# Kernel optimization log

Hardware: AMD Instinct MI355X
Metric: run time of the kernel (lower is better)

Reference implementation:

```python
import jax, jax.numpy as jnp
import numpy as np

N_NODES = 50000


def _gcn_conv(x, row, col, W, b, n_nodes):
    """PyG GCNConv: symmetric-normalized scatter-add aggregation.
    row/col already include self-loops. x: [N, Fin], W: [Fin, Fout]."""
    h = x @ W  # [N, Fout]
    deg = jax.ops.segment_sum(jnp.ones(col.shape[0], x.dtype), col,
                              num_segments=n_nodes)  # in-degree incl. self-loops
    dis = jnp.where(deg > 0, jax.lax.rsqrt(deg), 0.0)  # deg^{-1/2}
    norm = dis[row] * dis[col]  # [E+N]
    msg = h[row] * norm[:, None]  # gather + scale, [E+N, Fout]
    out = jax.ops.segment_sum(msg, col, num_segments=n_nodes)  # scatter-add
    return out + b


def setup_inputs() -> dict:
    key = jax.random.key(0)
    k1, k2, k3, k4 = jax.random.split(key, 4)
    N, E, FIN, FH = N_NODES, 800000, 512, 512
    x = jax.random.normal(k1, (N, FIN), dtype=jnp.float32)
    edge_index = jax.random.randint(k2, (2, E), 0, N, dtype=jnp.int64)
    W1 = jax.random.normal(k3, (FIN, FH), dtype=jnp.float32) * (1.0 / np.sqrt(FIN))
    b1 = jnp.zeros((FH,), jnp.float32)
    W2 = jax.random.normal(k4, (FH, FH), dtype=jnp.float32) * (1.0 / np.sqrt(FH))
    b2 = jnp.zeros((FH,), jnp.float32)
    return {"x": x, "edge_index": edge_index, "W1": W1, "b1": b1,
            "W2": W2, "b2": b2}


def reference(x, edge_index, W1, b1, W2, b2):
    n = x.shape[0]
    loops = jnp.arange(n, dtype=edge_index.dtype)
    row = jnp.concatenate([edge_index[0], loops])  # sources
    col = jnp.concatenate([edge_index[1], loops])  # targets
    h = _gcn_conv(x, row, col, W1, b1, n)
    h = jax.nn.relu(h)
    return _gcn_conv(h, row, col, W2, b2, n)
```

## Files before the change

kernel.cpp:

```cpp
#include <hip/hip_runtime.h>
#include <hip/hip_bf16.h>

typedef short short8 __attribute__((ext_vector_type(8)));
typedef unsigned short u16x8 __attribute__((ext_vector_type(8)));
typedef float f32x4 __attribute__((ext_vector_type(4)));

#define AS1 __attribute__((address_space(1)))
#define AS3 __attribute__((address_space(3)))

__device__ __forceinline__ void gload16(const void* g, void* l) {
  __builtin_amdgcn_global_load_lds((AS1 void*)g, (AS3 void*)l, 16, 0, 0);
}

__device__ __forceinline__ unsigned short f2bf(float f) {
  unsigned u = __float_as_uint(f);
  u = (u + 0x7FFF + ((u >> 16) & 1)) >> 16;
  return (unsigned short)u;
}
__device__ __forceinline__ float bf2f(unsigned short u) {
  return __uint_as_float(((unsigned)u) << 16);
}

__global__ void prep_kernel(const float4* __restrict__ x4, ushort4* __restrict__ xb4, int n4,
                            const float* __restrict__ W1, unsigned short* __restrict__ W1t,
                            const float* __restrict__ W2, unsigned short* __restrict__ W2t) {
  const int nthr = gridDim.x * 256;
  for (int i = blockIdx.x * 256 + threadIdx.x; i < n4; i += nthr) {
    float4 v = x4[i];
    ushort4 o;
    o.x = f2bf(v.x); o.y = f2bf(v.y); o.z = f2bf(v.z); o.w = f2bf(v.w);
    xb4[i] = o;
  }
  for (int idx = blockIdx.x * 256 + threadIdx.x; idx < 512 * 512; idx += nthr) {
    const int k = idx >> 9, n = idx & 511;
    W1t[n * 512 + k] = f2bf(W1[idx]);
    W2t[n * 512 + k] = f2bf(W2[idx]);
  }
}

__global__ void detect64_kernel(const int* __restrict__ ei32, int* __restrict__ flag) {
  const int lane = threadIdx.x;
  const int v = ei32[2 * lane + 1];
  const unsigned long long m = __ballot(v != 0);
  if (lane == 0) *flag = (m == 0ull) ? 1 : 0;
}

__global__ void count_kernel(const int* __restrict__ ei32, const int* __restrict__ flag,
                             int* __restrict__ cnt4, int E, int qdiv) {
  int e = blockIdx.x * 256 + threadIdx.x;
  if (e >= E) return;
  const int is64 = *flag;
  const int r = is64 ? ei32[2 * e] : ei32[e];
  const int c = is64 ? ei32[2 * E + 2 * e] : ei32[E + e];
  int q = r / qdiv; q = q > 3 ? 3 : q;
  atomicAdd(&cnt4[c * 4 + q], 1);
}

__global__ void __launch_bounds__(1024) scan_bsum_kernel(const int* __restrict__ cnt,
                                                         int* __restrict__ bsum, int n) {
  __shared__ int ws[16];
  const int tid = threadIdx.x, lane = tid & 63, wid = tid >> 6;
  const int i = blockIdx.x * 1024 + tid;
  int x = (i < n) ? cnt[i] : 0;
#pragma unroll
  for (int d = 1; d < 64; d <<= 1) x += __shfl_xor(x, d, 64);
  if (lane == 0) ws[wid] = x;
  __syncthreads();
  if (tid == 0) {
    int s = 0;
#pragma unroll
    for (int w = 0; w < 16; ++w) s += ws[w];
    bsum[blockIdx.x] = s;
  }
}

__global__ void __launch_bounds__(1024) scan_boff_kernel(int* __restrict__ bsum,
                                                         int* __restrict__ total, int B) {
  __shared__ int ws[16];
  const int tid = threadIdx.x, lane = tid & 63, wid = tid >> 6;
  const int v = (tid < B) ? bsum[tid] : 0;
  int x = v;
#pragma unroll
  for (int d = 1; d < 64; d <<= 1) {
    int y = __shfl_up(x, d, 64);
    if (lane >= d) x += y;
  }
  if (lane == 63) ws[wid] = x;
  __syncthreads();
  if (tid < 16) {
    int wv = ws[tid];
    int wx = wv;
#pragma unroll
    for (int d = 1; d < 16; d <<= 1) {
      int y = __shfl_up(wx, d, 64);
      if (tid >= d) wx += y;
    }
    ws[tid] = wx - wv;
  }
  __syncthreads();
  const int excl = ws[wid] + (x - v);
  if (tid < B) bsum[tid] = excl;
  if (tid == B - 1) *total = excl + v;
}

__global__ void __launch_bounds__(1024) scan_fill_kernel(const int* __restrict__ cnt,
    const int* __restrict__ boff, int* __restrict__ ptr, int* __restrict__ cur,
    float* __restrict__ dis, int n) {
  __shared__ int ws[16];
  const int tid = threadIdx.x, lane = tid & 63, wid = tid >> 6;
  const int j = blockIdx.x * 1024 + tid;
  const int v = (j < n) ? cnt[j] : 0;
  int x = v;
#pragma unroll
  for (int d = 1; d < 64; d <<= 1) {
    int y = __shfl_up(x, d, 64);
    if (lane >= d) x += y;
  }
  if (lane == 63) ws[wid] = x;
  __syncthreads();
  if (tid < 16) {
    int wv = ws[tid];
    int wx = wv;
#pragma unroll
    for (int d = 1; d < 16; d <<= 1) {
      int y = __shfl_up(wx, d, 64);
      if (tid >= d) wx += y;
    }
    ws[tid] = wx - wv;
  }
  __syncthreads();
  const int v1 = __shfl_down(v, 1, 64);
  const int v2 = __shfl_down(v, 2, 64);
  const int v3 = __shfl_down(v, 3, 64);
  if (j < n) {
    const int excl = boff[blockIdx.x] + ws[wid] + (x - v);
    ptr[j] = excl;
    cur[j] = excl;
    if ((j & 3) == 0) dis[j >> 2] = rsqrtf((float)(v + v1 + v2 + v3 + 1));
  }
}

__global__ void fill_kernel(const int* __restrict__ ei32, const int* __restrict__ flag,
                            int* __restrict__ cur4, int* __restrict__ eidx, int E, int qdiv) {
  int e = blockIdx.x * 256 + threadIdx.x;
  if (e >= E) return;
  const int is64 = *flag;
  const int r = is64 ? ei32[2 * e] : ei32[e];
  const int c = is64 ? ei32[2 * E + 2 * e] : ei32[E + e];
  int q = r / qdiv; q = q > 3 ? 3 : q;
  const int pos = atomicAdd(&cur4[c * 4 + q], 1);
  eidx[pos] = r;
}

template <bool BA, bool BC>
__global__ void __launch_bounds__(256, 3) gemm_kernel(const unsigned short* __restrict__ A,
                                                      const unsigned short* __restrict__ Bt,
                                                      const float* __restrict__ dscale,
                                                      unsigned short* __restrict__ C, int M) {
  __shared__ alignas(128) unsigned short As[8192];
  __shared__ alignas(128) unsigned short Bs[8192];
  const int tid = threadIdx.x;
  const int wave = tid >> 6, lane = tid & 63;
  const int wm = wave >> 1, wn = wave & 1;

  const int nbm = (M + 127) >> 7;
  const int nwg = nbm * 4;
  const int orig = blockIdx.x;
  const int xcd = orig & 7;
  const int q8 = nwg >> 3, r8 = nwg & 7;
  const int wg = (xcd < r8 ? xcd * (q8 + 1) : r8 * (q8 + 1) + (xcd - r8) * q8) + (orig >> 3);
  const int bn = wg & 3;
  const int bm = wg >> 2;

  const int lr = lane >> 3, ls = lane & 7;
  const int fr = lane & 15, ks = lane >> 4;

  f32x4 acc[4][4] = {};

#define STAGE(KO)                                                                          \
  {                                                                                        \
    _Pragma("unroll") for (int i = 0; i < 4; ++i) {                                        \
      int ra = bm * 128 + i * 32 + wave * 8 + lr;                                          \
      ra = ra < M ? ra : M - 1;                                                            \
      const size_t aoff = BA ? ((size_t)(KO)*M + (size_t)ra * 64 + ((ls ^ (lr & 7)) << 3)) \
                             : ((size_t)ra * 512 + (KO) + ((ls ^ (lr & 7)) << 3));         \
      gload16(A + aoff, &As[(i * 32 + wave * 8) * 64]);                                    \
      const int rb = bn * 128 + i * 32 + wave * 8 + lr;                                    \
      gload16(Bt + (size_t)rb * 512 + (KO) + ((ls ^ (lr & 7)) << 3),                       \
              &Bs[(i * 32 + wave * 8) * 64]);                                              \
    }                                                                                      \
  }

  for (int kt = 0; kt < 8; ++kt) {
    if (kt) __syncthreads();
    STAGE(kt * 64)
    __syncthreads();

#pragma unroll
    for (int kk = 0; kk < 2; ++kk) {
      short8 af[4], bfg[4];
#pragma unroll
      for (int m = 0; m < 4; ++m) {
        const int tr = wm * 64 + m * 16 + fr;
        af[m] = *(const short8*)&As[tr * 64 + ((ks * 8 + kk * 32) ^ ((tr & 7) << 3))];
      }
#pragma unroll
      for (int n = 0; n < 4; ++n) {
        const int tb = wn * 64 + n * 16 + fr;
        bfg[n] = *(const short8*)&Bs[tb * 64 + ((ks * 8 + kk * 32) ^ ((tb & 7) << 3))];
      }
#pragma unroll
      for (int m = 0; m < 4; ++m)
#pragma unroll
        for (int n = 0; n < 4; ++n)
          acc[m][n] = __builtin_amdgcn_mfma_f32_16x16x32_bf16(af[m], bfg[n], acc[m][n], 0, 0, 0);
    }
  }
#undef STAGE

  const int rbase = bm * 128 + wm * 64 + (lane >> 4) * 4;
  const int cbase = bn * 128 + wn * 64 + (lane & 15);
  const size_t hseg = (size_t)M * 64;
#pragma unroll
  for (int m = 0; m < 4; ++m)
#pragma unroll
    for (int j = 0; j < 4; ++j) {
      const int r = rbase + m * 16 + j;
      if (r < M) {
        const float ds = dscale[r];
#pragma unroll
        for (int n = 0; n < 4; ++n) {
          const unsigned short val = f2bf(acc[m][n][j] * ds);
          if (BC) {
            const int col = cbase + n * 16;
            C[(size_t)(col >> 6) * hseg + (size_t)r * 64 + (col & 63)] = val;
          } else {
            C[(size_t)r * 512 + cbase + n * 16] = val;
          }
        }
      }
    }
}

template <bool FINAL>
__global__ void __launch_bounds__(256) agg_kernel(const unsigned short* __restrict__ h,
    const int* __restrict__ eidx, const int* __restrict__ ptr4, const float* __restrict__ dis,
    const float* __restrict__ bias, void* __restrict__ outv, int n) {
  const int tid = threadIdx.x;
  const int lane = tid & 63;
  const int slice = blockIdx.x & 7;
  const int g = lane >> 3;
  const int c = lane & 7;
  const int node = (int)(blockIdx.x >> 3) * 32 + (tid >> 6) * 8 + g;
  if (node >= n) return;

  const unsigned short* hs = h + (size_t)slice * ((size_t)n * 64);
  const int coff = c * 8;

  const int start = ptr4[node * 4], end = ptr4[node * 4 + 4];
  float acc[8] = {0, 0, 0, 0, 0, 0, 0, 0};

  int e = start;
  for (; e + 2 <= end; e += 2) {
    const int s0 = eidx[e], s1 = eidx[e + 1];
    const u16x8 v0 = *(const u16x8*)(hs + (size_t)(unsigned)s0 * 64 + coff);
    const u16x8 v1 = *(const u16x8*)(hs + (size_t)(unsigned)s1 * 64 + coff);
#pragma unroll
    for (int j = 0; j < 8; ++j) acc[j] += bf2f(v0[j]) + bf2f(v1[j]);
  }
  if (e < end) {
    const int s0 = eidx[e];
    const u16x8 v = *(const u16x8*)(hs + (size_t)(unsigned)s0 * 64 + coff);
#pragma unroll
    for (int j = 0; j < 8; ++j) acc[j] += bf2f(v[j]);
  }

  {
    const u16x8 v = *(const u16x8*)(hs + (size_t)node * 64 + coff);
#pragma unroll
    for (int j = 0; j < 8; ++j) acc[j] += bf2f(v[j]);
  }

  const float di = dis[node];
  const int fcol = slice * 64 + coff;
  float b[8];
  *(float4*)&b[0] = *(const float4*)(bias + fcol);
  *(float4*)&b[4] = *(const float4*)(bias + fcol + 4);

  if (FINAL) {
    float* out = (float*)outv;
    float4 o0, o1;
    o0.x = acc[0] * di + b[0]; o0.y = acc[1] * di + b[1];
    o0.z = acc[2] * di + b[2]; o0.w = acc[3] * di + b[3];
    o1.x = acc[4] * di + b[4]; o1.y = acc[5] * di + b[5];
    o1.z = acc[6] * di + b[6]; o1.w = acc[7] * di + b[7];
    *(float4*)(out + (size_t)node * 512 + fcol) = o0;
    *(float4*)(out + (size_t)node * 512 + fcol + 4) = o1;
  } else {
    unsigned short* out = (unsigned short*)outv;
    u16x8 o;
#pragma unroll
    for (int j = 0; j < 8; ++j) {
      const float t = acc[j] * di + b[j];
      o[j] = f2bf(t > 0.0f ? t : 0.0f);
    }
    *(u16x8*)(out + (size_t)slice * ((size_t)n * 64) + (size_t)node * 64 + coff) = o;
  }
}

extern "C" void kernel_launch(void* const* d_in, const int* in_sizes, int n_in,
                              void* d_out, int out_size, void* d_ws, size_t ws_size,
                              hipStream_t stream) {
  const float* x  = (const float*)d_in[0];
  const int*   ei = (const int*)d_in[1];
  const float* W1 = (const float*)d_in[2];
  const float* b1 = (const float*)d_in[3];
  const float* W2 = (const float*)d_in[4];
  const float* b2 = (const float*)d_in[5];
  float* out = (float*)d_out;

  const int M = in_sizes[0] / 512;
  const int E = in_sizes[1] / 2;
  const int qdiv = (M + 3) >> 2;

  auto alignup = [](size_t v) { return (v + 255) & ~(size_t)255; };
  char* p = (char*)d_ws;
  unsigned short* xb  = (unsigned short*)p; p += alignup((size_t)M * 512 * 2);
  unsigned short* h1b = (unsigned short*)p; p += alignup((size_t)M * 512 * 2);
  unsigned short* r1b = (unsigned short*)p; p += alignup((size_t)M * 512 * 2);
  unsigned short* w1b = (unsigned short*)p; p += alignup(512 * 512 * 2);
  unsigned short* w2b = (unsigned short*)p; p += alignup(512 * 512 * 2);
  float* dis = (float*)p; p += alignup((size_t)M * 4);
  int* ptr4  = (int*)p;   p += alignup(((size_t)M * 4 + 1) * 4);
  int* eidx  = (int*)p;   p += alignup((size_t)E * 4);
  int* flag  = (int*)p;   p += alignup(256);
  int* bsum  = (int*)p;   p += alignup(1024);
  int* cnt4 = (int*)h1b;
  int* cur4 = (int*)((char*)h1b + alignup((size_t)M * 16));
  unsigned short* h2b = xb;

  const int n4 = M * 4;
  hipMemsetAsync(cnt4, 0, (size_t)n4 * 4, stream);
  detect64_kernel<<<1, 64, 0, stream>>>(ei, flag);

  prep_kernel<<<2048, 256, 0, stream>>>((const float4*)x, (ushort4*)xb, M * 128,
                                        W1, w1b, W2, w2b);

  const int B = (n4 + 1023) / 1024;
  count_kernel<<<(E + 255) / 256, 256, 0, stream>>>(ei, flag, cnt4, E, qdiv);
  scan_bsum_kernel<<<B, 1024, 0, stream>>>(cnt4, bsum, n4);
  scan_boff_kernel<<<1, 1024, 0, stream>>>(bsum, ptr4 + n4, B);
  scan_fill_kernel<<<B, 1024, 0, stream>>>(cnt4, bsum, ptr4, cur4, dis, n4);
  fill_kernel<<<(E + 255) / 256, 256, 0, stream>>>(ei, flag, cur4, eidx, E, qdiv);

  const int nwg = ((M + 127) / 128) * 4;
  const int nag = ((M + 31) / 32) * 8;
  gemm_kernel<false, true><<<nwg, 256, 0, stream>>>(xb, w1b, dis, h1b, M);
  agg_kernel<false><<<nag, 256, 0, stream>>>(h1b, eidx, ptr4, dis, b1, (void*)r1b, M);
  gemm_kernel<true, true><<<nwg, 256, 0, stream>>>(r1b, w2b, dis, h2b, M);
  agg_kernel<true><<<nag, 256, 0, stream>>>(h2b, eidx, ptr4, dis, b2, (void*)out, M);
}
```

Measured before the change: 380.3 us.

## Sort nodes by in-degree via histogram permutation to balance aggregation work

Builds a 64-bin in-degree histogram during the scan, prefix-scans it, and scatters node ids into a degree-sorted permutation. The aggregation kernels then process nodes in that order, so the 8 lanes-groups in a wave handle nodes with similar edge counts and divergence is reduced. It adds two small kernels, one memset and an extra indirection per node. Output writes become scattered rather than sequential, which can hurt locality.

```diff
diff --git a/kernel.cpp b/kernel.cpp
--- a/kernel.cpp
+++ b/kernel.cpp
@@ -105,9 +105,11 @@
 
 __global__ void __launch_bounds__(1024) scan_fill_kernel(const int* __restrict__ cnt,
     const int* __restrict__ boff, int* __restrict__ ptr, int* __restrict__ cur,
-    float* __restrict__ dis, int n) {
+    float* __restrict__ dis, int* __restrict__ hist, int n) {
   __shared__ int ws[16];
+  __shared__ int lhist[64];
   const int tid = threadIdx.x, lane = tid & 63, wid = tid >> 6;
+  if (tid < 64) lhist[tid] = 0;
   const int j = blockIdx.x * 1024 + tid;
   const int v = (j < n) ? cnt[j] : 0;
   int x = v;
@@ -136,8 +138,35 @@
     const int excl = boff[blockIdx.x] + ws[wid] + (x - v);
     ptr[j] = excl;
     cur[j] = excl;
-    if ((j & 3) == 0) dis[j >> 2] = rsqrtf((float)(v + v1 + v2 + v3 + 1));
-  }
+    if ((j & 3) == 0) {
+      const int deg = v + v1 + v2 + v3;
+      dis[j >> 2] = rsqrtf((float)(deg + 1));
+      atomicAdd(&lhist[deg > 63 ? 63 : deg], 1);
+    }
+  }
+  __syncthreads();
+  if (tid < 64 && lhist[tid]) atomicAdd(&hist[tid], lhist[tid]);
+}
+
+__global__ void hist_scan_kernel(const int* __restrict__ hist, int* __restrict__ hcur) {
+  const int lane = threadIdx.x;
+  const int v = hist[lane];
+  int x = v;
+#pragma unroll
+  for (int d = 1; d < 64; d <<= 1) {
+    int y = __shfl_up(x, d, 64);
+    if (lane >= d) x += y;
+  }
+  hcur[lane] = x - v;
+}
+
+__global__ void scatter_perm_kernel(const int* __restrict__ ptr4, int* __restrict__ hcur,
+                                    int* __restrict__ perm, int n) {
+  const int i = blockIdx.x * 256 + threadIdx.x;
+  if (i >= n) return;
+  const int deg = ptr4[i * 4 + 4] - ptr4[i * 4];
+  const int pos = atomicAdd(&hcur[deg > 63 ? 63 : deg], 1);
+  perm[pos] = i;
 }
 
 __global__ void fill_kernel(const int* __restrict__ ei32, const int* __restrict__ flag,
@@ -245,14 +274,16 @@
 template <bool FINAL>
 __global__ void __launch_bounds__(256) agg_kernel(const unsigned short* __restrict__ h,
     const int* __restrict__ eidx, const int* __restrict__ ptr4, const float* __restrict__ dis,
-    const float* __restrict__ bias, void* __restrict__ outv, int n) {
+    const int* __restrict__ perm, const float* __restrict__ bias, void* __restrict__ outv,
+    int n) {
   const int tid = threadIdx.x;
   const int lane = tid & 63;
   const int slice = blockIdx.x & 7;
   const int g = lane >> 3;
   const int c = lane & 7;
-  const int node = (int)(blockIdx.x >> 3) * 32 + (tid >> 6) * 8 + g;
-  if (node >= n) return;
+  const int rank = (int)(blockIdx.x >> 3) * 32 + (tid >> 6) * 8 + g;
+  if (rank >= n) return;
+  const int node = perm[rank];
 
   const unsigned short* hs = h + (size_t)slice * ((size_t)n * 64);
   const int coff = c * 8;
@@ -333,14 +364,18 @@
   float* dis = (float*)p; p += alignup((size_t)M * 4);
   int* ptr4  = (int*)p;   p += alignup(((size_t)M * 4 + 1) * 4);
   int* eidx  = (int*)p;   p += alignup((size_t)E * 4);
+  int* perm  = (int*)p;   p += alignup((size_t)M * 4);
   int* flag  = (int*)p;   p += alignup(256);
   int* bsum  = (int*)p;   p += alignup(1024);
+  int* hist  = (int*)p;   p += alignup(256);
+  int* hcur  = (int*)p;   p += alignup(256);
   int* cnt4 = (int*)h1b;
   int* cur4 = (int*)((char*)h1b + alignup((size_t)M * 16));
   unsigned short* h2b = xb;
 
   const int n4 = M * 4;
   hipMemsetAsync(cnt4, 0, (size_t)n4 * 4, stream);
+  hipMemsetAsync(hist, 0, 256, stream);
   detect64_kernel<<<1, 64, 0, stream>>>(ei, flag);
 
   prep_kernel<<<2048, 256, 0, stream>>>((const float4*)x, (ushort4*)xb, M * 128,
@@ -350,13 +385,15 @@
   count_kernel<<<(E + 255) / 256, 256, 0, stream>>>(ei, flag, cnt4, E, qdiv);
   scan_bsum_kernel<<<B, 1024, 0, stream>>>(cnt4, bsum, n4);
   scan_boff_kernel<<<1, 1024, 0, stream>>>(bsum, ptr4 + n4, B);
-  scan_fill_kernel<<<B, 1024, 0, stream>>>(cnt4, bsum, ptr4, cur4, dis, n4);
+  scan_fill_kernel<<<B, 1024, 0, stream>>>(cnt4, bsum, ptr4, cur4, dis, hist, n4);
   fill_kernel<<<(E + 255) / 256, 256, 0, stream>>>(ei, flag, cur4, eidx, E, qdiv);
+  hist_scan_kernel<<<1, 64, 0, stream>>>(hist, hcur);
+  scatter_perm_kernel<<<(M + 255) / 256, 256, 0, stream>>>(ptr4, hcur, perm, M);
 
   const int nwg = ((M + 127) / 128) * 4;
   const int nag = ((M + 31) / 32) * 8;
   gemm_kernel<false, true><<<nwg, 256, 0, stream>>>(xb, w1b, dis, h1b, M);
-  agg_kernel<false><<<nag, 256, 0, stream>>>(h1b, eidx, ptr4, dis, b1, (void*)r1b, M);
+  agg_kernel<false><<<nag, 256, 0, stream>>>(h1b, eidx, ptr4, dis, perm, b1, (void*)r1b, M);
   gemm_kernel<true, true><<<nwg, 256, 0, stream>>>(r1b, w2b, dis, h2b, M);
-  agg_kernel<true><<<nag, 256, 0, stream>>>(h2b, eidx, ptr4, dis, b2, (void*)out, M);
-}
+  agg_kernel<true><<<nag, 256, 0, stream>>>(h2b, eidx, ptr4, dis, perm, b2, (void*)out, M);
+}
```

New measurement: 543.5 us. +42.9%, slower.

## Make GEMM persistent with the full B column panel resident in LDS

Applied to the files above, without the earlier changes.

The GEMM becomes a persistent kernel with 256 blocks of 512 threads. Each block loads its entire 128x512 slice of the transposed weight into LDS once (128 KB), then loops over row tiles, streaming A through registers into LDS with a one-step prefetch. This removes the repeated weight loads per tile and the per-tile block launch cost. In exchange, occupancy drops to one block per CU, A staging goes through registers with full vmcnt waits, and the loop keeps one barrier per k-step.

```diff
diff --git a/kernel.cpp b/kernel.cpp
--- a/kernel.cpp
+++ b/kernel.cpp
@@ -153,93 +153,102 @@
 }
 
 template <bool BA, bool BC>
-__global__ void __launch_bounds__(256, 3) gemm_kernel(const unsigned short* __restrict__ A,
-                                                      const unsigned short* __restrict__ Bt,
-                                                      const float* __restrict__ dscale,
-                                                      unsigned short* __restrict__ C, int M) {
-  __shared__ alignas(128) unsigned short As[8192];
-  __shared__ alignas(128) unsigned short Bs[8192];
+__global__ void __launch_bounds__(512, 1) gemm_pb_kernel(const unsigned short* __restrict__ A,
+    const unsigned short* __restrict__ Bt, const float* __restrict__ dscale,
+    unsigned short* __restrict__ C, int M) {
+  __shared__ alignas(128) unsigned short Bs[128 * 512];
+  __shared__ alignas(128) unsigned short As[128 * 64];
   const int tid = threadIdx.x;
   const int wave = tid >> 6, lane = tid & 63;
-  const int wm = wave >> 1, wn = wave & 1;
-
+  const int wm = wave >> 2, wn = wave & 3;
+  const int fr = lane & 15, ks = lane >> 4;
   const int nbm = (M + 127) >> 7;
-  const int nwg = nbm * 4;
-  const int orig = blockIdx.x;
-  const int xcd = orig & 7;
-  const int q8 = nwg >> 3, r8 = nwg & 7;
-  const int wg = (xcd < r8 ? xcd * (q8 + 1) : r8 * (q8 + 1) + (xcd - r8) * q8) + (orig >> 3);
-  const int bn = wg & 3;
-  const int bm = wg >> 2;
-
-  const int lr = lane >> 3, ls = lane & 7;
-  const int fr = lane & 15, ks = lane >> 4;
-
-  f32x4 acc[4][4] = {};
-
-#define STAGE(KO)                                                                          \
-  {                                                                                        \
-    _Pragma("unroll") for (int i = 0; i < 4; ++i) {                                        \
-      int ra = bm * 128 + i * 32 + wave * 8 + lr;                                          \
-      ra = ra < M ? ra : M - 1;                                                            \
-      const size_t aoff = BA ? ((size_t)(KO)*M + (size_t)ra * 64 + ((ls ^ (lr & 7)) << 3)) \
-                             : ((size_t)ra * 512 + (KO) + ((ls ^ (lr & 7)) << 3));         \
-      gload16(A + aoff, &As[(i * 32 + wave * 8) * 64]);                                    \
-      const int rb = bn * 128 + i * 32 + wave * 8 + lr;                                    \
-      gload16(Bt + (size_t)rb * 512 + (KO) + ((ls ^ (lr & 7)) << 3),                       \
-              &Bs[(i * 32 + wave * 8) * 64]);                                              \
-    }                                                                                      \
-  }
-
-  for (int kt = 0; kt < 8; ++kt) {
-    if (kt) __syncthreads();
-    STAGE(kt * 64)
-    __syncthreads();
-
-#pragma unroll
-    for (int kk = 0; kk < 2; ++kk) {
-      short8 af[4], bfg[4];
-#pragma unroll
-      for (int m = 0; m < 4; ++m) {
-        const int tr = wm * 64 + m * 16 + fr;
-        af[m] = *(const short8*)&As[tr * 64 + ((ks * 8 + kk * 32) ^ ((tr & 7) << 3))];
+  const size_t seg = (size_t)M * 64;
+
+  const int xcd = blockIdx.x & 7, j = blockIdx.x >> 3;
+  const int bn = j & 3, row0 = j >> 3 == 0 ? (j >> 2) : (j >> 2);
+  const int r0 = j >> 2;
+
+  for (int i = 0; i < 16; ++i) {
+    const int cc = wave + i * 8;
+    const int ssl = (lane & 56) | ((lane & 7) ^ (cc & 7));
+    gload16(Bt + (size_t)(bn * 128 + cc) * 512 + ssl * 8, &Bs[cc * 512]);
+  }
+
+  const int arow = tid >> 2;
+  const int asl = (tid & 3) * 2;
+
+  for (int bm = xcd + 8 * r0; bm < nbm; bm += 64) {
+    int ra = bm * 128 + arow;
+    ra = ra < M ? ra : M - 1;
+    const unsigned short* abase = BA ? (A + (size_t)ra * 64) : (A + (size_t)ra * 512);
+
+    u16x8 ar0, ar1;
+    {
+      const unsigned short* s = abase;
+      ar0 = *(const u16x8*)(s + asl * 8);
+      ar1 = *(const u16x8*)(s + asl * 8 + 8);
+    }
+
+    f32x4 acc[4][2] = {};
+
+    for (int kt = 0; kt < 8; ++kt) {
+      asm volatile("s_waitcnt vmcnt(0)" ::: "memory");
+      __builtin_amdgcn_s_barrier();
+      asm volatile("" ::: "memory");
+      *(u16x8*)&As[arow * 64 + ((asl)     ^ (arow & 7)) * 8] = ar0;
+      *(u16x8*)&As[arow * 64 + ((asl + 1) ^ (arow & 7)) * 8] = ar1;
+      if (kt < 7) {
+        const unsigned short* s = BA ? (abase + (size_t)(kt + 1) * seg)
+                                     : (abase + (kt + 1) * 64);
+        ar0 = *(const u16x8*)(s + asl * 8);
+        ar1 = *(const u16x8*)(s + asl * 8 + 8);
       }
-#pragma unroll
-      for (int n = 0; n < 4; ++n) {
-        const int tb = wn * 64 + n * 16 + fr;
-        bfg[n] = *(const short8*)&Bs[tb * 64 + ((ks * 8 + kk * 32) ^ ((tb & 7) << 3))];
+      asm volatile("s_waitcnt lgkmcnt(0)" ::: "memory");
+      __builtin_amdgcn_s_barrier();
+      asm volatile("" ::: "memory");
+
+#pragma unroll
+      for (int kk = 0; kk < 2; ++kk) {
+        short8 af[4], bf[2];
+#pragma unroll
+        for (int m = 0; m < 4; ++m) {
+          const int tr = wm * 64 + m * 16 + fr;
+          af[m] = *(const short8*)&As[tr * 64 + (((kk * 4 + ks) ^ (tr & 7)) * 8)];
+        }
+#pragma unroll
+        for (int n = 0; n < 2; ++n) {
+          const int tb = wn * 32 + n * 16 + fr;
+          const int g = kt * 8 + kk * 4 + ks;
+          bf[n] = *(const short8*)&Bs[tb * 512 + (((g & 56) | ((g & 7) ^ (tb & 7))) * 8)];
+        }
+#pragma unroll
+        for (int m = 0; m < 4; ++m)
+#pragma unroll
+          for (int n = 0; n < 2; ++n)
+            acc[m][n] = __builtin_amdgcn_mfma_f32_16x16x32_bf16(af[m], bf[n], acc[m][n], 0, 0, 0);
       }
-#pragma unroll
-      for (int m = 0; m < 4; ++m)
-#pragma unroll
-        for (int n = 0; n < 4; ++n)
-          acc[m][n] = __builtin_amdgcn_mfma_f32_16x16x32_bf16(af[m], bfg[n], acc[m][n], 0, 0, 0);
-    }
-  }
-#undef STAGE
-
-  const int rbase = bm * 128 + wm * 64 + (lane >> 4) * 4;
-  const int cbase = bn * 128 + wn * 64 + (lane & 15);
-  const size_t hseg = (size_t)M * 64;
-#pragma unroll
-  for (int m = 0; m < 4; ++m)
-#pragma unroll
-    for (int j = 0; j < 4; ++j) {
-      const int r = rbase + m * 16 + j;
-      if (r < M) {
-        const float ds = dscale[r];
-#pragma unroll
-        for (int n = 0; n < 4; ++n) {
-          const unsigned short val = f2bf(acc[m][n][j] * ds);
-          if (BC) {
-            const int col = cbase + n * 16;
-            C[(size_t)(col >> 6) * hseg + (size_t)r * 64 + (col & 63)] = val;
-          } else {
-            C[(size_t)r * 512 + cbase + n * 16] = val;
+    }
+
+    const int rbase = bm * 128 + wm * 64 + (lane >> 4) * 4;
+    const int cb = bn * 128 + wn * 32 + (lane & 15);
+#pragma unroll
+    for (int m = 0; m < 4; ++m)
+#pragma unroll
+      for (int jj = 0; jj < 4; ++jj) {
+        const int r = rbase + m * 16 + jj;
+        if (r < M) {
+          const float ds = dscale[r];
+#pragma unroll
+          for (int n = 0; n < 2; ++n) {
+            const int col = cb + n * 16;
+            const unsigned short val = f2bf(acc[m][n][jj] * ds);
+            if (BC) C[(size_t)(col >> 6) * seg + (size_t)r * 64 + (col & 63)] = val;
+            else    C[(size_t)r * 512 + col] = val;
           }
         }
       }
-    }
+  }
 }
 
 template <bool FINAL>
@@ -353,10 +362,9 @@
   scan_fill_kernel<<<B, 1024, 0, stream>>>(cnt4, bsum, ptr4, cur4, dis, n4);
   fill_kernel<<<(E + 255) / 256, 256, 0, stream>>>(ei, flag, cur4, eidx, E, qdiv);
 
-  const int nwg = ((M + 127) / 128) * 4;
   const int nag = ((M + 31) / 32) * 8;
-  gemm_kernel<false, true><<<nwg, 256, 0, stream>>>(xb, w1b, dis, h1b, M);
+  gemm_pb_kernel<false, true><<<256, 512, 0, stream>>>(xb, w1b, dis, h1b, M);
   agg_kernel<false><<<nag, 256, 0, stream>>>(h1b, eidx, ptr4, dis, b1, (void*)r1b, M);
-  gemm_kernel<true, true><<<nwg, 256, 0, stream>>>(r1b, w2b, dis, h2b, M);
+  gemm_pb_kernel<true, true><<<256, 512, 0, stream>>>(r1b, w2b, dis, h2b, M);
   agg_kernel<true><<<nag, 256, 0, stream>>>(h2b, eidx, ptr4, dis, b2, (void*)out, M);
 }
```

Measured after the change: 416.3 us. 1.09x slower.
